# Kernel optimization log

Measured on AMD Instinct MI355X. Metric: run time of the kernel, lower is better.

## Reference

```python
import jax, jax.numpy as jnp
import numpy as np

N_NODES = 50000   # local subgraph nodes
N_ENT   = 100000  # global entity vocab
N_REL   = 16
DIM     = 128
LAYERS  = 2
E       = 600000  # edges
Q       = 8192    # query triples
PATH_DIM = 5
RULE_INIT = [[1.0, 1.0, 0.5, 0.0, 0.0], [0.0, 0.0, 0.0, 1.0, 1.0]]


def setup_inputs() -> dict:
    key = jax.random.key(0)
    ks = jax.random.split(key, 11)
    node_ids   = jax.random.randint(ks[0], (N_NODES,), 0, N_ENT)
    edge_index = jax.random.randint(ks[1], (2, E), 0, N_NODES)
    edge_type  = jax.random.randint(ks[2], (E,), 0, N_REL)
    heads = jax.random.randint(ks[3], (Q,), 0, N_NODES)
    rels  = jax.random.randint(ks[4], (Q,), 0, N_REL)
    tails = jax.random.randint(ks[5], (Q,), 0, N_NODES)
    path_feat = jax.random.normal(ks[6], (Q, PATH_DIM), dtype=jnp.float32)
    # learned parameters
    entity_emb = jax.random.normal(ks[7], (N_ENT, DIM), dtype=jnp.float32) * 0.1
    rel_emb    = jax.random.normal(ks[8], (N_REL, DIM), dtype=jnp.float32) * 0.1
    W_self = jax.random.normal(ks[9], (LAYERS, DIM, DIM), dtype=jnp.float32) / np.sqrt(DIM)
    W_rel  = jax.random.normal(ks[10], (LAYERS, N_REL, DIM, DIM), dtype=jnp.float32) / np.sqrt(DIM)
    delta_weight = jnp.zeros((2, PATH_DIM), dtype=jnp.float32)
    lambda_logit = jnp.zeros((2,), dtype=jnp.float32)
    rule_init_weight = jnp.asarray(RULE_INIT, dtype=jnp.float32)
    return {
        'node_ids': node_ids, 'edge_index': edge_index, 'edge_type': edge_type,
        'heads': heads, 'rels': rels, 'tails': tails,
        'path_feat': path_feat, 'rel_task_idx': 0,
        'entity_emb': entity_emb, 'rel_emb': rel_emb,
        'W_self': W_self, 'W_rel': W_rel,
        'delta_weight': delta_weight, 'lambda_logit': lambda_logit,
        'rule_init_weight': rule_init_weight,
    }


def _rgcn_layer(h, Ws, Wr, src, dst, etype):
    # relation-specific transforms for all nodes: [R, N, D]
    h_rel = jnp.einsum('nd,rde->rne', h, Wr)
    msgs = h_rel[etype, src]                    # [E, D] gather per edge
    # per-(dst, relation) mean normalization (standard RGCN 1/c_{i,r})
    seg = dst * N_REL + etype
    cnt = jax.ops.segment_sum(jnp.ones((E,), h.dtype), seg, num_segments=N_NODES * N_REL)
    msgs = msgs / jnp.maximum(cnt[seg], 1.0)[:, None]
    agg = jax.ops.segment_sum(msgs, dst, num_segments=N_NODES)  # [N, D]
    return jax.nn.relu(h @ Ws + agg)


def reference(node_ids, edge_index, edge_type, heads, rels, tails, path_feat,
              rel_task_idx, entity_emb, rel_emb, W_self, W_rel,
              delta_weight, lambda_logit, rule_init_weight):
    src, dst = edge_index[0], edge_index[1]
    h = entity_emb[node_ids]                      # [N, D] local node states
    for l in range(LAYERS):
        h = _rgcn_layer(h, W_self[l], W_rel[l], src, dst, edge_type)
    # DistMult scoring of query triples (local indices)
    score_graph = jnp.sum(h[heads] * rel_emb[rels] * h[tails], axis=-1)  # [Q]
    # path branch
    final_weight = rule_init_weight[rel_task_idx] + delta_weight[rel_task_idx]  # [PATH_DIM]
    score_path = path_feat @ final_weight                                # [Q]
    lam = jax.nn.sigmoid(lambda_logit[rel_task_idx])
    return lam * score_graph + (1.0 - lam) * score_path
```

## Files before the change

### kernel.cpp

```cpp
#include <hip/hip_runtime.h>

#define N_NODES 50000
#define N_ENT   100000
#define N_REL   16
#define DIM     128
#define E_EDGES 600000
#define NQ      8192
#define PATH_DIM 5
#define NK      (N_NODES * N_REL)
#define NBLK_SEG (NK / 256)
#define KTOT    (N_REL * DIM + DIM)
#define NG      (KTOT / 32)
#define BM      32
#define EB      ((E_EDGES + 255) / 256)
#define H0B     ((N_NODES * 32) / 256)
#define WCB     ((2 * NG * 8 * 512) / 256)

typedef __attribute__((ext_vector_type(8))) short short8;
typedef __attribute__((ext_vector_type(4))) float floatx4;
typedef __attribute__((ext_vector_type(4))) unsigned uintx4;

static __device__ __forceinline__ short f2bf(float x) {
  unsigned u = __builtin_bit_cast(unsigned, x);
  u = (u + 0x7FFFu + ((u >> 16) & 1u)) >> 16;
  return (short)u;
}
static __device__ __forceinline__ float bf_lo(unsigned u) {
  return __builtin_bit_cast(float, u << 16);
}
static __device__ __forceinline__ float bf_hi(unsigned u) {
  return __builtin_bit_cast(float, u & 0xffff0000u);
}
static __device__ __forceinline__ unsigned pk2(float a, float b) {
  return (unsigned)(unsigned short)f2bf(a) | ((unsigned)(unsigned short)f2bf(b) << 16);
}

static __device__ __forceinline__ int wave_incl_scan(int x) {
  int lane = threadIdx.x & 63;
  #pragma unroll
  for (int off = 1; off < 64; off <<= 1) {
    int y = __shfl_up(x, off, 64);
    if (lane >= off) x += y;
  }
  return x;
}

__global__ void k_prep(const int* __restrict__ ei, const int* __restrict__ et,
                       int* __restrict__ hist,
                       const int* __restrict__ nid, const float* __restrict__ emb,
                       unsigned* __restrict__ h,
                       const float* __restrict__ wrel, const float* __restrict__ wself,
                       short* __restrict__ wt) {
  int b = blockIdx.x, t = threadIdx.x;
  if (b < EB) {
    int e = b * 256 + t;
    if (e < E_EDGES) {
      int key = et[e] * N_NODES + ei[E_EDGES + e];
      atomicAdd(&hist[key], 1);
    }
  } else if (b < EB + H0B) {
    int g = (b - EB) * 256 + t;
    int n = g >> 5, q = g & 31;
    float4 v = *(const float4*)(emb + (size_t)nid[n] * DIM + q * 4);
    uint2 pk;
    pk.x = pk2(v.x, v.y);
    pk.y = pk2(v.z, v.w);
    *(uint2*)(h + (size_t)n * 64 + q * 2) = pk;
  } else {
    int idx = (b - EB - H0B) * 256 + t;
    int u = idx & 511;
    int tile = idx >> 9;
    int rA = u & 15, q = u >> 4;
    int nt8 = tile & 7;
    int lg = tile >> 3;
    int l = lg / NG, g = lg % NG;
    int n = nt8 * 16 + rA;
    int k = g * 32 + q;
    float v;
    if (k < N_REL * DIM) {
      int r = k >> 7, d = k & 127;
      v = wrel[(((size_t)l * N_REL + r) * DIM + d) * DIM + n];
    } else {
      int d = k - N_REL * DIM;
      v = wself[((size_t)l * DIM + d) * DIM + n];
    }
    wt[(size_t)tile * 512 + rA * 32 + q] = f2bf(v);
  }
}

__global__ void k_bsum(const int* __restrict__ hist, int* __restrict__ bsum) {
  int t = threadIdx.x;
  int v = hist[blockIdx.x * 256 + t];
  #pragma unroll
  for (int off = 32; off; off >>= 1) v += __shfl_xor(v, off, 64);
  __shared__ int s4[4];
  if ((t & 63) == 0) s4[t >> 6] = v;
  __syncthreads();
  if (t == 0) bsum[blockIdx.x] = s4[0] + s4[1] + s4[2] + s4[3];
}

__global__ void k_offsets(const int* __restrict__ hist, const int* __restrict__ bsum,
                          int* __restrict__ offs, int* __restrict__ cursor) {
  int t = threadIdx.x;
  int b = blockIdx.x;
  int g = b * 256 + t;
  int part = 0;
  for (int i = t; i < b; i += 256) part += bsum[i];
  #pragma unroll
  for (int off = 32; off; off >>= 1) part += __shfl_xor(part, off, 64);
  __shared__ int pre4[4];
  int wid = t >> 6, lane = t & 63;
  if (lane == 0) pre4[wid] = part;
  __syncthreads();
  int blockpre = pre4[0] + pre4[1] + pre4[2] + pre4[3];

  int v = hist[g];
  int incl = wave_incl_scan(v);
  __shared__ int wsum[4];
  if (lane == 63) wsum[wid] = incl;
  __syncthreads();
  int wexcl = 0;
  for (int i = 0; i < wid; i++) wexcl += wsum[i];
  int off = blockpre + wexcl + incl - v;
  offs[g] = off;
  cursor[g] = off;
  if (g == NK - 1) offs[NK] = off + v;
}

__global__ void k_scatter(const int* __restrict__ ei, const int* __restrict__ et,
                          int* __restrict__ cursor, int* __restrict__ ssrc) {
  int e = blockIdx.x * 256 + threadIdx.x;
  if (e >= E_EDGES) return;
  int src = ei[e];
  int key = et[e] * N_NODES + ei[E_EDGES + e];
  int pos = atomicAdd(&cursor[key], 1);
  ssrc[pos] = src;
}

__global__ __launch_bounds__(256, 4)
void k_layer(const unsigned* __restrict__ hin, const int* __restrict__ offs,
             const int* __restrict__ ssrc, const short* __restrict__ wt,
             unsigned* __restrict__ hout) {
  __shared__ int offsS[16][40];
  __shared__ float cred[2][32][64];
  int t = threadIdx.x;
  int w = t >> 6, lane = t & 63;
  int quad = lane >> 4, rA = lane & 15;
  int rg = w >> 1, kg = w & 1;
  int row0 = blockIdx.x * BM;
  int rbase = row0 + rg * 16;
  int rg16 = rg * 16;

  for (int idx = t; idx < 16 * 40; idx += 256) {
    int r = idx / 40, j = idx - r * 40;
    if (j < 33) offsS[r][j] = offs[min(r * N_NODES + row0 + j, NK)];
  }
  __syncthreads();

  floatx4 acc[8];
  #pragma unroll
  for (int nt = 0; nt < 8; ++nt) acc[nt] = (floatx4)0.f;

  const short* hb = (const short*)hin;

  int rlo = kg * 8, rhi = rlo + 8;
  for (int r = rlo; r < rhi; ++r) {
    int o = offsS[r][rg16 + rA];
    int c = offsS[r][rg16 + rA + 1] - o;
    int mc = c;
    #pragma unroll
    for (int sh = 32; sh; sh >>= 1) mc = max(mc, __shfl_xor(mc, sh, 64));
    float s[4][8];
    #pragma unroll
    for (int ks = 0; ks < 4; ++ks)
      #pragma unroll
      for (int m = 0; m < 8; ++m) s[ks][m] = 0.f;
    int eid = (c > 0) ? ssrc[o] : 0;
    for (int i = 0; i < mc; ++i) {
      int eidn = (i + 1 < c) ? ssrc[o + i + 1] : 0;
      if (i < c) {
        const short* hp = hb + (size_t)eid * DIM + quad * 8;
        #pragma unroll
        for (int ks = 0; ks < 4; ++ks) {
          uint4 d = *(const uint4*)(hp + ks * 32);
          s[ks][0] += bf_lo(d.x); s[ks][1] += bf_hi(d.x);
          s[ks][2] += bf_lo(d.y); s[ks][3] += bf_hi(d.y);
          s[ks][4] += bf_lo(d.z); s[ks][5] += bf_hi(d.z);
          s[ks][6] += bf_lo(d.w); s[ks][7] += bf_hi(d.w);
        }
      }
      eid = eidn;
    }
    float inv = 1.0f / (float)(c > 0 ? c : 1);
    #pragma unroll
    for (int ks = 0; ks < 4; ++ks) {
      uintx4 ap;
      #pragma unroll
      for (int m = 0; m < 4; ++m) {
        float a = s[ks][2 * m] * inv, b = s[ks][2 * m + 1] * inv;
        unsigned pk;
        asm("v_cvt_pk_bf16_f32 %0, %1, %2" : "=v"(pk) : "v"(a), "v"(b));
        ap[m] = pk;
      }
      short8 af = __builtin_bit_cast(short8, ap);
      const short* bp = wt + (size_t)((r * 4 + ks) * 8) * 512 + rA * 32 + quad * 8;
      #pragma unroll
      for (int nt = 0; nt < 8; ++nt) {
        short8 b = *(const short8*)(bp + nt * 512);
        acc[nt] = __builtin_amdgcn_mfma_f32_16x16x32_bf16(af, b, acc[nt], 0, 0, 0);
      }
    }
  }

  if (kg == 1) {
    int lr = min(rbase + rA, N_NODES - 1);
    const short* hp = hb + (size_t)lr * DIM + quad * 8;
    #pragma unroll
    for (int ks = 0; ks < 4; ++ks) {
      short8 af = *(const short8*)(hp + ks * 32);
      const short* bp = wt + (size_t)((16 * 4 + ks) * 8) * 512 + rA * 32 + quad * 8;
      #pragma unroll
      for (int nt = 0; nt < 8; ++nt) {
        short8 b = *(const short8*)(bp + nt * 512);
        acc[nt] = __builtin_amdgcn_mfma_f32_16x16x32_bf16(af, b, acc[nt], 0, 0, 0);
      }
    }
    #pragma unroll
    for (int nt = 0; nt < 8; ++nt)
      #pragma unroll
      for (int j = 0; j < 4; ++j)
        cred[rg][nt * 4 + j][lane] = acc[nt][j];
  }
  __syncthreads();
  if (kg == 0) {
    #pragma unroll
    for (int nt = 0; nt < 8; ++nt)
      #pragma unroll
      for (int j = 0; j < 4; ++j) {
        float v = acc[nt][j] + cred[rg][nt * 4 + j][lane];
        int row = rbase + quad * 4 + j;
        int col = nt * 16 + rA;
        if (row < N_NODES)
          ((short*)hout)[(size_t)row * DIM + col] = f2bf(fmaxf(v, 0.f));
      }
  }
}

__global__ void k_score(const unsigned* __restrict__ h, const int* __restrict__ heads,
                        const int* __restrict__ rels, const int* __restrict__ tails,
                        const float* __restrict__ rel_emb, const float* __restrict__ path_feat,
                        const int* __restrict__ task_idx, const float* __restrict__ delta_w,
                        const float* __restrict__ lambda_logit, const float* __restrict__ rule_init,
                        float* __restrict__ out) {
  int q = (blockIdx.x * 256 + threadIdx.x) >> 6;
  int lane = threadIdx.x & 63;
  int hd = heads[q], tl = tails[q], rl = rels[q];
  unsigned ua = h[(size_t)hd * 64 + lane];
  unsigned uc = h[(size_t)tl * 64 + lane];
  float2 r = *(const float2*)(rel_emb + (size_t)rl * DIM + lane * 2);
  float s = bf_lo(ua) * r.x * bf_lo(uc) + bf_hi(ua) * r.y * bf_hi(uc);
  #pragma unroll
  for (int off = 32; off; off >>= 1) s += __shfl_xor(s, off, 64);
  if (lane == 0) {
    int task = task_idx[0];
    float sp = 0.f;
    #pragma unroll
    for (int p = 0; p < PATH_DIM; p++)
      sp += path_feat[q * PATH_DIM + p] *
            (rule_init[task * PATH_DIM + p] + delta_w[task * PATH_DIM + p]);
    float lam = 1.f / (1.f + __expf(-lambda_logit[task]));
    out[q] = lam * s + (1.f - lam) * sp;
  }
}

extern "C" void kernel_launch(void* const* d_in, const int* in_sizes, int n_in,
                              void* d_out, int out_size, void* d_ws, size_t ws_size,
                              hipStream_t stream) {
  const int*   node_ids   = (const int*)d_in[0];
  const int*   edge_index = (const int*)d_in[1];
  const int*   edge_type  = (const int*)d_in[2];
  const int*   heads      = (const int*)d_in[3];
  const int*   rels       = (const int*)d_in[4];
  const int*   tails      = (const int*)d_in[5];
  const float* path_feat  = (const float*)d_in[6];
  const int*   task_idx   = (const int*)d_in[7];
  const float* entity_emb = (const float*)d_in[8];
  const float* rel_emb    = (const float*)d_in[9];
  const float* W_self     = (const float*)d_in[10];
  const float* W_rel      = (const float*)d_in[11];
  const float* delta_w    = (const float*)d_in[12];
  const float* lambda_lg  = (const float*)d_in[13];
  const float* rule_init  = (const float*)d_in[14];

  char* ws = (char*)d_ws;
  size_t off = 0;
  auto alloc = [&](size_t bytes) -> void* {
    void* p = ws + off;
    off = (off + bytes + 255) & ~(size_t)255;
    return p;
  };
  unsigned* h_a    = (unsigned*)alloc((size_t)N_NODES * DIM * 2);
  unsigned* h_b    = (unsigned*)alloc((size_t)N_NODES * DIM * 2);
  short*    wt     = (short*)alloc((size_t)2 * NG * 8 * 512 * 2);
  int*      offs   = (int*)alloc((size_t)(NK + 1) * 4);
  int*      ssrc   = (int*)alloc((size_t)E_EDGES * 4);
  int*      hist   = (int*)alloc((size_t)(NK + 1) * 4);
  int*      cursor = (int*)alloc((size_t)NK * 4);
  int*      bsum   = (int*)alloc((size_t)NBLK_SEG * 4);

  hipMemsetAsync(hist, 0, (size_t)(NK + 1) * 4, stream);
  k_prep<<<EB + H0B + WCB, 256, 0, stream>>>(edge_index, edge_type, hist,
                                             node_ids, entity_emb, h_a,
                                             W_rel, W_self, wt);
  k_bsum<<<NBLK_SEG, 256, 0, stream>>>(hist, bsum);
  k_offsets<<<NBLK_SEG, 256, 0, stream>>>(hist, bsum, offs, cursor);
  k_scatter<<<EB, 256, 0, stream>>>(edge_index, edge_type, cursor, ssrc);

  const unsigned* hin = h_a;
  unsigned* hout = h_b;
  int nblk = (N_NODES + BM - 1) / BM;
  for (int l = 0; l < 2; l++) {
    k_layer<<<nblk, 256, 0, stream>>>(hin, offs, ssrc,
                                      wt + (size_t)l * NG * 8 * 512, hout);
    const unsigned* tmp = hout;
    hout = (unsigned*)hin;
    hin = tmp;
  }
  k_score<<<NQ / 4, 256, 0, stream>>>(hin, heads, rels, tails, rel_emb, path_feat,
                                      task_idx, delta_w, lambda_lg, rule_init,
                                      (float*)d_out);
}
```

Baseline: 497.2 us.

## Double rows per warp in RGCN layer to reuse weight fragments across two MFMA tiles

Raises the block row tile from 32 to 64 so each warp handles two 16-row groups and issues two MFMAs per loaded weight fragment. Weight-fragment global loads per output row are halved. In exchange it doubles accumulator registers and LDS for the cross-warp reduction, and lowers launch bounds to 2 blocks per CU, which reduces occupancy for the latency-bound neighbour gather loop. Each warp now runs its two gathers one after the other, so per-warp gather latency grows.

New measurement: 528.1 us. 6.2% more time.

```diff
diff --git a/kernel.cpp b/kernel.cpp
--- a/kernel.cpp
+++ b/kernel.cpp
@@ -11,7 +11,7 @@
 #define NBLK_SEG (NK / 256)
 #define KTOT    (N_REL * DIM + DIM)
 #define NG      (KTOT / 32)
-#define BM      32
+#define BM      64
 #define EB      ((E_EDGES + 255) / 256)
 #define H0B     ((N_NODES * 32) / 256)
 #define WCB     ((2 * NG * 8 * 512) / 256)
@@ -137,112 +137,132 @@
   ssrc[pos] = src;
 }
 
-__global__ __launch_bounds__(256, 4)
+__global__ __launch_bounds__(256, 2)
 void k_layer(const unsigned* __restrict__ hin, const int* __restrict__ offs,
              const int* __restrict__ ssrc, const short* __restrict__ wt,
              unsigned* __restrict__ hout) {
-  __shared__ int offsS[16][40];
-  __shared__ float cred[2][32][64];
+  __shared__ int offsS[16][68];
+  __shared__ float cred[2][2][32][64];
   int t = threadIdx.x;
   int w = t >> 6, lane = t & 63;
   int quad = lane >> 4, rA = lane & 15;
-  int rg = w >> 1, kg = w & 1;
+  int kg = w & 1, rg = w >> 1;
   int row0 = blockIdx.x * BM;
-  int rbase = row0 + rg * 16;
-  int rg16 = rg * 16;
-
-  for (int idx = t; idx < 16 * 40; idx += 256) {
-    int r = idx / 40, j = idx - r * 40;
-    if (j < 33) offsS[r][j] = offs[min(r * N_NODES + row0 + j, NK)];
-  }
-  __syncthreads();
-
-  floatx4 acc[8];
-  #pragma unroll
-  for (int nt = 0; nt < 8; ++nt) acc[nt] = (floatx4)0.f;
+  int rbase = row0 + rg * 32;
+  int rb32 = rg * 32;
+
+  for (int idx = t; idx < 16 * 80; idx += 256) {
+    int r = idx / 80, j = idx - r * 80;
+    if (j < 65) offsS[r][j] = offs[min(r * N_NODES + row0 + j, NK)];
+  }
+  __syncthreads();
+
+  floatx4 acc[2][8];
+  #pragma unroll
+  for (int g = 0; g < 2; ++g)
+    #pragma unroll
+    for (int nt = 0; nt < 8; ++nt) acc[g][nt] = (floatx4)0.f;
 
   const short* hb = (const short*)hin;
 
   int rlo = kg * 8, rhi = rlo + 8;
   for (int r = rlo; r < rhi; ++r) {
-    int o = offsS[r][rg16 + rA];
-    int c = offsS[r][rg16 + rA + 1] - o;
-    int mc = c;
-    #pragma unroll
-    for (int sh = 32; sh; sh >>= 1) mc = max(mc, __shfl_xor(mc, sh, 64));
-    float s[4][8];
-    #pragma unroll
-    for (int ks = 0; ks < 4; ++ks)
-      #pragma unroll
-      for (int m = 0; m < 8; ++m) s[ks][m] = 0.f;
-    int eid = (c > 0) ? ssrc[o] : 0;
-    for (int i = 0; i < mc; ++i) {
-      int eidn = (i + 1 < c) ? ssrc[o + i + 1] : 0;
-      if (i < c) {
-        const short* hp = hb + (size_t)eid * DIM + quad * 8;
+    short8 af[2][4];
+    #pragma unroll
+    for (int g = 0; g < 2; ++g) {
+      int o = offsS[r][rb32 + g * 16 + rA];
+      int c = offsS[r][rb32 + g * 16 + rA + 1] - o;
+      int mc = c;
+      #pragma unroll
+      for (int sh = 32; sh; sh >>= 1) mc = max(mc, __shfl_xor(mc, sh, 64));
+      float s[4][8];
+      #pragma unroll
+      for (int ks = 0; ks < 4; ++ks)
         #pragma unroll
-        for (int ks = 0; ks < 4; ++ks) {
-          uint4 d = *(const uint4*)(hp + ks * 32);
-          s[ks][0] += bf_lo(d.x); s[ks][1] += bf_hi(d.x);
-          s[ks][2] += bf_lo(d.y); s[ks][3] += bf_hi(d.y);
-          s[ks][4] += bf_lo(d.z); s[ks][5] += bf_hi(d.z);
-          s[ks][6] += bf_lo(d.w); s[ks][7] += bf_hi(d.w);
+        for (int m = 0; m < 8; ++m) s[ks][m] = 0.f;
+      int eid = (c > 0) ? ssrc[o] : 0;
+      for (int i = 0; i < mc; ++i) {
+        int eidn = (i + 1 < c) ? ssrc[o + i + 1] : 0;
+        if (i < c) {
+          const short* hp = hb + (size_t)eid * DIM + quad * 8;
+          #pragma unroll
+          for (int ks = 0; ks < 4; ++ks) {
+            uint4 d = *(const uint4*)(hp + ks * 32);
+            s[ks][0] += bf_lo(d.x); s[ks][1] += bf_hi(d.x);
+            s[ks][2] += bf_lo(d.y); s[ks][3] += bf_hi(d.y);
+            s[ks][4] += bf_lo(d.z); s[ks][5] += bf_hi(d.z);
+            s[ks][6] += bf_lo(d.w); s[ks][7] += bf_hi(d.w);
+          }
         }
+        eid = eidn;
       }
-      eid = eidn;
-    }
-    float inv = 1.0f / (float)(c > 0 ? c : 1);
+      float inv = 1.0f / (float)(c > 0 ? c : 1);
+      #pragma unroll
+      for (int ks = 0; ks < 4; ++ks) {
+        uintx4 ap;
+        #pragma unroll
+        for (int m = 0; m < 4; ++m) {
+          float a = s[ks][2 * m] * inv, b = s[ks][2 * m + 1] * inv;
+          unsigned pk;
+          asm("v_cvt_pk_bf16_f32 %0, %1, %2" : "=v"(pk) : "v"(a), "v"(b));
+          ap[m] = pk;
+        }
+        af[g][ks] = __builtin_bit_cast(short8, ap);
+      }
+    }
     #pragma unroll
     for (int ks = 0; ks < 4; ++ks) {
-      uintx4 ap;
-      #pragma unroll
-      for (int m = 0; m < 4; ++m) {
-        float a = s[ks][2 * m] * inv, b = s[ks][2 * m + 1] * inv;
-        unsigned pk;
-        asm("v_cvt_pk_bf16_f32 %0, %1, %2" : "=v"(pk) : "v"(a), "v"(b));
-        ap[m] = pk;
-      }
-      short8 af = __builtin_bit_cast(short8, ap);
       const short* bp = wt + (size_t)((r * 4 + ks) * 8) * 512 + rA * 32 + quad * 8;
       #pragma unroll
       for (int nt = 0; nt < 8; ++nt) {
         short8 b = *(const short8*)(bp + nt * 512);
-        acc[nt] = __builtin_amdgcn_mfma_f32_16x16x32_bf16(af, b, acc[nt], 0, 0, 0);
+        acc[0][nt] = __builtin_amdgcn_mfma_f32_16x16x32_bf16(af[0][ks], b, acc[0][nt], 0, 0, 0);
+        acc[1][nt] = __builtin_amdgcn_mfma_f32_16x16x32_bf16(af[1][ks], b, acc[1][nt], 0, 0, 0);
       }
     }
   }
 
   if (kg == 1) {
-    int lr = min(rbase + rA, N_NODES - 1);
-    const short* hp = hb + (size_t)lr * DIM + quad * 8;
+    short8 af[2][4];
+    #pragma unroll
+    for (int g = 0; g < 2; ++g) {
+      int lr = min(rbase + g * 16 + rA, N_NODES - 1);
+      const short* hp = hb + (size_t)lr * DIM + quad * 8;
+      #pragma unroll
+      for (int ks = 0; ks < 4; ++ks) af[g][ks] = *(const short8*)(hp + ks * 32);
+    }
     #pragma unroll
     for (int ks = 0; ks < 4; ++ks) {
-      short8 af = *(const short8*)(hp + ks * 32);
       const short* bp = wt + (size_t)((16 * 4 + ks) * 8) * 512 + rA * 32 + quad * 8;
       #pragma unroll
       for (int nt = 0; nt < 8; ++nt) {
         short8 b = *(const short8*)(bp + nt * 512);
-        acc[nt] = __builtin_amdgcn_mfma_f32_16x16x32_bf16(af, b, acc[nt], 0, 0, 0);
+        acc[0][nt] = __builtin_amdgcn_mfma_f32_16x16x32_bf16(af[0][ks], b, acc[0][nt], 0, 0, 0);
+        acc[1][nt] = __builtin_amdgcn_mfma_f32_16x16x32_bf16(af[1][ks], b, acc[1][nt], 0, 0, 0);
       }
     }
     #pragma unroll
-    for (int nt = 0; nt < 8; ++nt)
-      #pragma unroll
-      for (int j = 0; j < 4; ++j)
-        cred[rg][nt * 4 + j][lane] = acc[nt][j];
+    for (int g = 0; g < 2; ++g)
+      #pragma unroll
+      for (int nt = 0; nt < 8; ++nt)
+        #pragma unroll
+        for (int j = 0; j < 4; ++j)
+          cred[rg][g][nt * 4 + j][lane] = acc[g][nt][j];
   }
   __syncthreads();
   if (kg == 0) {
     #pragma unroll
-    for (int nt = 0; nt < 8; ++nt)
-      #pragma unroll
-      for (int j = 0; j < 4; ++j) {
-        float v = acc[nt][j] + cred[rg][nt * 4 + j][lane];
-        int row = rbase + quad * 4 + j;
-        int col = nt * 16 + rA;
-        if (row < N_NODES)
-          ((short*)hout)[(size_t)row * DIM + col] = f2bf(fmaxf(v, 0.f));
-      }
+    for (int g = 0; g < 2; ++g)
+      #pragma unroll
+      for (int nt = 0; nt < 8; ++nt)
+        #pragma unroll
+        for (int j = 0; j < 4; ++j) {
+          float v = acc[g][nt][j] + cred[rg][g][nt * 4 + j][lane];
+          int row = rbase + g * 16 + quad * 4 + j;
+          int col = nt * 16 + rA;
+          if (row < N_NODES)
+            ((short*)hout)[(size_t)row * DIM + col] = f2bf(fmaxf(v, 0.f));
+        }
   }
 }
 
```
